# Performance work log

Hardware: AMD Instinct MI355X
Metric: run time of the kernel (lower is better)

The kernel has to match this reference:

```python
import jax, jax.numpy as jnp
import numpy as np

NH = 16  # matches init kwarg nh


def setup_inputs() -> dict:
    key = jax.random.key(0)
    k1, k2 = jax.random.split(key)
    b, S, T = 4, 4096, 4096
    x = jax.random.normal(k1, (b, S, 1), dtype=jnp.float32)
    coords_rel = jax.random.normal(k2, (2, b, S, T), dtype=jnp.float32)
    return {"x": x, "coords_rel": coords_rel}


def reference(x, coords_rel):
    # coords_rel: [2, b, S, T]; x: [b, S, 1]
    d = jnp.sqrt(coords_rel[0] ** 2 + coords_rel[1] ** 2)            # [b, S, T]
    # torch.topk(d, NH, dim=1, largest=False): smallest NH along source dim, ascending
    neg_vals, idx = jax.lax.top_k(jnp.transpose(-d, (0, 2, 1)), NH)  # [b, T, NH]
    dist_abs = jnp.transpose(-neg_vals, (0, 2, 1))                   # [b, NH, T]
    indices = jnp.transpose(idx, (0, 2, 1))                          # [b, NH, T]
    b, nh, t = dist_abs.shape
    w = 1.0 / (dist_abs + 1e-15) ** 2                                # [b, nh, t]
    denom = w.sum(axis=2)                                            # [b, nh] (sum over t, as in source)
    # faithful reproduction of torch .view(t,b,nh) raw reinterpretation + broadcast divide + .view(b,t,nh)
    w = (w.reshape(t, b, nh) / denom).reshape(b, t, nh)              # [b, t, nh]
    S = x.shape[1]
    idx_btn = indices.reshape(b, t, nh)                              # raw reshape, matches torch .view
    # gather: out[i,j,k] = x[i, idx[i,j,k], 0]  (x.repeat over last dim makes all columns equal)
    xg = jnp.take_along_axis(jnp.broadcast_to(x, (b, S, nh)), idx_btn, axis=1)  # [b, t, nh]
    out = (xg * w).sum(axis=2)                                       # [b, t]
    return out[..., None]                                            # [b, t, 1]
```

## Files before the change

kernel.cpp:

```cpp
#include <hip/hip_runtime.h>

#define B_ 4
#define S_ 4096
#define T_ 4096
#define NH_ 16
#define CPB 32
#define CPW 2
#define ROWS 64
#define NTILE (S_ / ROWS)
#define LDSP 33
#define NCG (T_ / CPB)

typedef unsigned long long u64;

__global__ __launch_bounds__(1024, 8) void topk_scan(
    const float* __restrict__ coords,
    float* __restrict__ outW,
    int*   __restrict__ outI,
    float* __restrict__ partials)
{
    __shared__ float lds0[ROWS * LDSP];
    __shared__ float lds1[ROWS * LDSP];
    __shared__ float red[16 * NH_];

    const int bid  = blockIdx.x;
    const int b    = bid >> 7;
    const int c0   = (bid & (NCG - 1)) * CPB;
    const int tid  = threadIdx.x;
    const int w    = tid >> 6;
    const int lane = tid & 63;

    const size_t plane = (size_t)B_ * S_ * T_;
    const int stid = tid & 511;
    const int srow = stid >> 3;
    const int scol = (stid & 7) * 4;
    const float* gp = coords + (size_t)b * S_ * T_ + (size_t)srow * T_ + (c0 + scol)
                    + (tid >= 512 ? plane : (size_t)0);
    float* ldsw = (tid >= 512 ? lds1 : lds0) + srow * LDSP + scol;

    float lv[CPW]; int li[CPW]; float tau[CPW];
#pragma unroll
    for (int cc = 0; cc < CPW; ++cc) {
        lv[cc]  = __int_as_float(0x7f800000);
        li[cc]  = 0;
        tau[cc] = __int_as_float(0x7f800000);
    }

    float4 v4 = *(const float4*)gp;

#pragma unroll 1
    for (int k = 0; k < NTILE; ++k) {
        __syncthreads();
        ldsw[0] = v4.x; ldsw[1] = v4.y; ldsw[2] = v4.z; ldsw[3] = v4.w;
        if (k + 1 < NTILE)
            v4 = *(const float4*)(gp + (size_t)(k + 1) * ROWS * T_);
        __syncthreads();

#pragma unroll
        for (int cc = 0; cc < CPW; ++cc) {
            const int col = w * CPW + cc;
            const float dx = lds0[lane * LDSP + col];
            const float dy = lds1[lane * LDSP + col];
            const float d2 = __fadd_rn(__fmul_rn(dx, dx), __fmul_rn(dy, dy));
            u64 m = __ballot(d2 < tau[cc]);
            while (m) {
                const int src = __ffsll(m) - 1;
                m &= m - 1;
                const float cd = __shfl(d2, src);
                const int   ci = k * ROWS + src;
                const unsigned pm = (unsigned)__ballot(lv[cc] <= cd) & 0xFFFFu;
                const int p = __popc(pm);
                const float uv = __shfl_up(lv[cc], 1);
                const int   ui = __shfl_up(li[cc], 1);
                const bool here  = (lane == p);
                const bool shift = (lane > p) && (lane < NH_);
                lv[cc] = here ? cd : (shift ? uv : lv[cc]);
                li[cc] = here ? ci : (shift ? ui : li[cc]);
                tau[cc] = __shfl(lv[cc], NH_ - 1);
                m &= __ballot(d2 < tau[cc]);
            }
        }
    }

    float dsum = 0.f;
#pragma unroll
    for (int cc = 0; cc < CPW; ++cc) {
        const int t = c0 + w * CPW + cc;
        if (lane < NH_) {
            const float d = sqrtf(lv[cc]) + 1e-15f;
            const float wv = 1.0f / (d * d);
            outW[((size_t)b * T_ + t) * NH_ + lane] = wv;
            outI[((size_t)b * T_ + t) * NH_ + lane] = li[cc];
            dsum += wv;
        }
    }
    if (lane < NH_) red[w * NH_ + lane] = dsum;
    __syncthreads();
    if (tid < NH_) {
        float s = 0.f;
#pragma unroll
        for (int q = 0; q < 16; ++q) s += red[q * NH_ + tid];
        partials[(size_t)bid * NH_ + tid] = s;
    }
}

__global__ __launch_bounds__(64) void denom_reduce(
    const float* __restrict__ partials, float* __restrict__ denom)
{
    const int q = threadIdx.x;
    const int b = q >> 4, j = q & 15;
    float s = 0.f;
    for (int g = 0; g < NCG; ++g)
        s += partials[(size_t)(b * NCG + g) * NH_ + j];
    denom[q] = s;
}

__global__ __launch_bounds__(256) void out_kernel(
    const float* __restrict__ x,
    const float* __restrict__ outW,
    const int*   __restrict__ outI,
    const float* __restrict__ denom,
    float* __restrict__ out)
{
    const int gid = blockIdx.x * 256 + threadIdx.x;
    const int i = gid >> 12;
    const int j = gid & 4095;
    const int ih = j >> 8;
    const size_t base = ((size_t)i * T_ + (size_t)(j & 255) * NH_) * NH_ + ih;
    const int dq = (j & 3) * NH_;
    float acc = 0.f;
#pragma unroll
    for (int k = 0; k < NH_; ++k) {
        float w  = outW[base + (size_t)k * NH_];
        int   id = outI[base + (size_t)k * NH_];
        acc += x[i * S_ + id] * w / denom[dq + k];
    }
    out[gid] = acc;
}

extern "C" void kernel_launch(void* const* d_in, const int* in_sizes, int n_in,
                              void* d_out, int out_size, void* d_ws, size_t ws_size,
                              hipStream_t stream) {
    const float* x      = (const float*)d_in[0];
    const float* coords = (const float*)d_in[1];
    float* out = (float*)d_out;

    float* outW     = (float*)d_ws;
    int*   outI     = (int*)(outW + (size_t)B_ * T_ * NH_);
    float* partials = (float*)(outI + (size_t)B_ * T_ * NH_);
    float* denom    = partials + (size_t)(B_ * NCG) * NH_;

    topk_scan   <<<B_ * NCG,      1024, 0, stream>>>(coords, outW, outI, partials);
    denom_reduce<<<1,             64,   0, stream>>>(partials, denom);
    out_kernel  <<<B_ * T_ / 256, 256,  0, stream>>>(x, outW, outI, denom, out);
}
```

Baseline: 155.3 us.

## Double-buffer LDS tiles in topk scan and parallelize denominator reduction

Result: faster. 152.1 us (-2.1%).

```diff
diff --git a/kernel.cpp b/kernel.cpp
--- a/kernel.cpp
+++ b/kernel.cpp
@@ -19,8 +19,7 @@
     int*   __restrict__ outI,
     float* __restrict__ partials)
 {
-    __shared__ float lds0[ROWS * LDSP];
-    __shared__ float lds1[ROWS * LDSP];
+    __shared__ float lds[2][2][ROWS * LDSP];
     __shared__ float red[16 * NH_];
 
     const int bid  = blockIdx.x;
@@ -34,9 +33,11 @@
     const int stid = tid & 511;
     const int srow = stid >> 3;
     const int scol = (stid & 7) * 4;
+    const int pl   = (tid >= 512) ? 1 : 0;
     const float* gp = coords + (size_t)b * S_ * T_ + (size_t)srow * T_ + (c0 + scol)
-                    + (tid >= 512 ? plane : (size_t)0);
-    float* ldsw = (tid >= 512 ? lds1 : lds0) + srow * LDSP + scol;
+                    + (pl ? plane : (size_t)0);
+    float* w0 = &lds[0][pl][srow * LDSP + scol];
+    float* w1 = &lds[1][pl][srow * LDSP + scol];
 
     float lv[CPW]; int li[CPW]; float tau[CPW];
 #pragma unroll
@@ -46,21 +47,27 @@
         tau[cc] = __int_as_float(0x7f800000);
     }
 
-    float4 v4 = *(const float4*)gp;
+    float4 r4 = *(const float4*)gp;
+    w0[0] = r4.x; w0[1] = r4.y; w0[2] = r4.z; w0[3] = r4.w;
+    r4 = *(const float4*)(gp + (size_t)ROWS * T_);
+    __syncthreads();
 
 #pragma unroll 1
     for (int k = 0; k < NTILE; ++k) {
-        __syncthreads();
-        ldsw[0] = v4.x; ldsw[1] = v4.y; ldsw[2] = v4.z; ldsw[3] = v4.w;
-        if (k + 1 < NTILE)
-            v4 = *(const float4*)(gp + (size_t)(k + 1) * ROWS * T_);
-        __syncthreads();
+        if (k + 1 < NTILE) {
+            float* wb = (k & 1) ? w0 : w1;
+            wb[0] = r4.x; wb[1] = r4.y; wb[2] = r4.z; wb[3] = r4.w;
+        }
+        if (k + 2 < NTILE)
+            r4 = *(const float4*)(gp + (size_t)(k + 2) * ROWS * T_);
 
+        const float* rb0 = lds[k & 1][0];
+        const float* rb1 = lds[k & 1][1];
 #pragma unroll
         for (int cc = 0; cc < CPW; ++cc) {
             const int col = w * CPW + cc;
-            const float dx = lds0[lane * LDSP + col];
-            const float dy = lds1[lane * LDSP + col];
+            const float dx = rb0[lane * LDSP + col];
+            const float dy = rb1[lane * LDSP + col];
             const float d2 = __fadd_rn(__fmul_rn(dx, dx), __fmul_rn(dy, dy));
             u64 m = __ballot(d2 < tau[cc]);
             while (m) {
@@ -80,6 +87,7 @@
                 m &= __ballot(d2 < tau[cc]);
             }
         }
+        __syncthreads();
     }
 
     float dsum = 0.f;
@@ -104,15 +112,20 @@
     }
 }
 
-__global__ __launch_bounds__(64) void denom_reduce(
+__global__ __launch_bounds__(128) void denom_reduce(
     const float* __restrict__ partials, float* __restrict__ denom)
 {
-    const int q = threadIdx.x;
+    const int q = blockIdx.x;
     const int b = q >> 4, j = q & 15;
-    float s = 0.f;
-    for (int g = 0; g < NCG; ++g)
-        s += partials[(size_t)(b * NCG + g) * NH_ + j];
-    denom[q] = s;
+    const int g = threadIdx.x;
+    __shared__ float sm[128];
+    sm[g] = partials[(size_t)(b * NCG + g) * NH_ + j];
+    __syncthreads();
+    for (int s = 64; s > 0; s >>= 1) {
+        if (g < s) sm[g] += sm[g + s];
+        __syncthreads();
+    }
+    if (g == 0) denom[q] = sm[0];
 }
 
 __global__ __launch_bounds__(256) void out_kernel(
@@ -151,6 +164,6 @@
     float* denom    = partials + (size_t)(B_ * NCG) * NH_;
 
     topk_scan   <<<B_ * NCG,      1024, 0, stream>>>(coords, outW, outI, partials);
-    denom_reduce<<<1,             64,   0, stream>>>(partials, denom);
+    denom_reduce<<<64,            128,  0, stream>>>(partials, denom);
     out_kernel  <<<B_ * T_ / 256, 256,  0, stream>>>(x, outW, outI, denom, out);
 }
```

## Split top-k scan across source spans with merge kernel and double-buffered LDS

Applied to the files above, without the earlier changes.

Measured after the change: 212.9 us. 1.37x slower.

```diff
diff --git a/kernel.cpp b/kernel.cpp
--- a/kernel.cpp
+++ b/kernel.cpp
@@ -4,39 +4,42 @@
 #define S_ 4096
 #define T_ 4096
 #define NH_ 16
-#define CPB 32
-#define CPW 2
+#define CPB 64
+#define CPW 4
 #define ROWS 64
-#define NTILE (S_ / ROWS)
-#define LDSP 33
+#define SSPAN 2048
+#define NSPAN 2
+#define NT (SSPAN / ROWS)
+#define LDSP 65
 #define NCG (T_ / CPB)
 
 typedef unsigned long long u64;
 
 __global__ __launch_bounds__(1024, 8) void topk_scan(
     const float* __restrict__ coords,
-    float* __restrict__ outW,
-    int*   __restrict__ outI,
-    float* __restrict__ partials)
-{
-    __shared__ float lds0[ROWS * LDSP];
-    __shared__ float lds1[ROWS * LDSP];
-    __shared__ float red[16 * NH_];
+    float* __restrict__ pv,
+    unsigned short* __restrict__ pi)
+{
+    __shared__ float lds[2][ROWS * LDSP];
 
     const int bid  = blockIdx.x;
     const int b    = bid >> 7;
-    const int c0   = (bid & (NCG - 1)) * CPB;
+    const int rem  = bid & 127;
+    const int cgl  = rem >> 1;
+    const int span = rem & 1;
     const int tid  = threadIdx.x;
     const int w    = tid >> 6;
     const int lane = tid & 63;
 
     const size_t plane = (size_t)B_ * S_ * T_;
-    const int stid = tid & 511;
-    const int srow = stid >> 3;
-    const int scol = (stid & 7) * 4;
-    const float* gp = coords + (size_t)b * S_ * T_ + (size_t)srow * T_ + (c0 + scol)
-                    + (tid >= 512 ? plane : (size_t)0);
-    float* ldsw = (tid >= 512 ? lds1 : lds0) + srow * LDSP + scol;
+    const int srow = tid >> 4;
+    const int scol = (tid & 15) * 4;
+    const int c0   = cgl * CPB;
+    const int s0   = span * SSPAN;
+    const float* g0 = coords + (size_t)b * S_ * T_ + (size_t)(s0 + srow) * T_ + (c0 + scol);
+    const float* g1 = g0 + plane;
+    float* w0 = &lds[0][srow * LDSP + scol];
+    float* w1 = &lds[1][srow * LDSP + scol];
 
     float lv[CPW]; int li[CPW]; float tau[CPW];
 #pragma unroll
@@ -46,28 +49,44 @@
         tau[cc] = __int_as_float(0x7f800000);
     }
 
-    float4 v4 = *(const float4*)gp;
+    float4 ax = *(const float4*)g0;
+    float4 ay = *(const float4*)g1;
+    w0[0] = __fadd_rn(__fmul_rn(ax.x, ax.x), __fmul_rn(ay.x, ay.x));
+    w0[1] = __fadd_rn(__fmul_rn(ax.y, ax.y), __fmul_rn(ay.y, ay.y));
+    w0[2] = __fadd_rn(__fmul_rn(ax.z, ax.z), __fmul_rn(ay.z, ay.z));
+    w0[3] = __fadd_rn(__fmul_rn(ax.w, ax.w), __fmul_rn(ay.w, ay.w));
+    ax = *(const float4*)(g0 + (size_t)ROWS * T_);
+    ay = *(const float4*)(g1 + (size_t)ROWS * T_);
+    __syncthreads();
 
 #pragma unroll 1
-    for (int k = 0; k < NTILE; ++k) {
-        __syncthreads();
-        ldsw[0] = v4.x; ldsw[1] = v4.y; ldsw[2] = v4.z; ldsw[3] = v4.w;
-        if (k + 1 < NTILE)
-            v4 = *(const float4*)(gp + (size_t)(k + 1) * ROWS * T_);
-        __syncthreads();
-
+    for (int k = 0; k < NT; ++k) {
+        if (k + 1 < NT) {
+            float* wb = (k & 1) ? w0 : w1;
+            wb[0] = __fadd_rn(__fmul_rn(ax.x, ax.x), __fmul_rn(ay.x, ay.x));
+            wb[1] = __fadd_rn(__fmul_rn(ax.y, ax.y), __fmul_rn(ay.y, ay.y));
+            wb[2] = __fadd_rn(__fmul_rn(ax.z, ax.z), __fmul_rn(ay.z, ay.z));
+            wb[3] = __fadd_rn(__fmul_rn(ax.w, ax.w), __fmul_rn(ay.w, ay.w));
+        }
+        if (k + 2 < NT) {
+            ax = *(const float4*)(g0 + (size_t)(k + 2) * ROWS * T_);
+            ay = *(const float4*)(g1 + (size_t)(k + 2) * ROWS * T_);
+        }
+
+        const float* rb = lds[k & 1];
+        float d2v[CPW];
+#pragma unroll
+        for (int cc = 0; cc < CPW; ++cc)
+            d2v[cc] = rb[lane * LDSP + (w * CPW + cc)];
 #pragma unroll
         for (int cc = 0; cc < CPW; ++cc) {
-            const int col = w * CPW + cc;
-            const float dx = lds0[lane * LDSP + col];
-            const float dy = lds1[lane * LDSP + col];
-            const float d2 = __fadd_rn(__fmul_rn(dx, dx), __fmul_rn(dy, dy));
+            const float d2 = d2v[cc];
             u64 m = __ballot(d2 < tau[cc]);
             while (m) {
                 const int src = __ffsll(m) - 1;
                 m &= m - 1;
                 const float cd = __shfl(d2, src);
-                const int   ci = k * ROWS + src;
+                const int   ci = s0 + k * ROWS + src;
                 const unsigned pm = (unsigned)__ballot(lv[cc] <= cd) & 0xFFFFu;
                 const int p = __popc(pm);
                 const float uv = __shfl_up(lv[cc], 1);
@@ -80,27 +99,68 @@
                 m &= __ballot(d2 < tau[cc]);
             }
         }
-    }
-
-    float dsum = 0.f;
+        __syncthreads();
+    }
+
 #pragma unroll
     for (int cc = 0; cc < CPW; ++cc) {
-        const int t = c0 + w * CPW + cc;
         if (lane < NH_) {
-            const float d = sqrtf(lv[cc]) + 1e-15f;
-            const float wv = 1.0f / (d * d);
-            outW[((size_t)b * T_ + t) * NH_ + lane] = wv;
-            outI[((size_t)b * T_ + t) * NH_ + lane] = li[cc];
-            dsum += wv;
-        }
-    }
-    if (lane < NH_) red[w * NH_ + lane] = dsum;
+            const size_t base = ((size_t)bid * NH_ + lane) * 64 + (w * CPW + cc);
+            pv[base] = lv[cc];
+            pi[base] = (unsigned short)li[cc];
+        }
+    }
+}
+
+__global__ __launch_bounds__(256) void topk_merge(
+    const float* __restrict__ pv, const unsigned short* __restrict__ pi,
+    float* __restrict__ outW,
+    int*   __restrict__ outI,
+    float* __restrict__ partials)
+{
+    __shared__ float red[NH_ * 257];
+
+    const int gc  = blockIdx.x * 256 + threadIdx.x;
+    const int b   = gc >> 12;
+    const int t   = gc & 4095;
+    const int cgl = t >> 6;
+    const int cl  = t & 63;
+    const int bid0 = ((b << 6) | cgl) << 1;
+
+    float cv[NH_]; int ci[NH_];
+#pragma unroll
+    for (int j = 0; j < NH_; ++j) { cv[j] = __int_as_float(0x7f800000); ci[j] = 0; }
+
+    for (int sp = 0; sp < NSPAN; ++sp) {
+        const size_t base = ((size_t)(bid0 + sp) * NH_) * 64 + cl;
+        for (int j = 0; j < NH_; ++j) {
+            float v = pv[base + (size_t)j * 64];
+            if (!(v < cv[NH_ - 1])) break;
+            int vi = (int)pi[base + (size_t)j * 64];
+#pragma unroll
+            for (int q = 0; q < NH_; ++q) {
+                bool sw = v < cv[q];
+                float tv = cv[q]; int ti = ci[q];
+                cv[q] = sw ? v : tv;  ci[q] = sw ? vi : ti;
+                v = sw ? tv : v;      vi = sw ? ti : vi;
+            }
+        }
+    }
+
+    const size_t obase = (size_t)gc * NH_;
+#pragma unroll
+    for (int j = 0; j < NH_; ++j) {
+        const float d = sqrtf(cv[j]) + 1e-15f;
+        const float wv = 1.0f / (d * d);
+        outW[obase + j] = wv;
+        outI[obase + j] = ci[j];
+        red[j * 257 + threadIdx.x] = wv;
+    }
     __syncthreads();
-    if (tid < NH_) {
+    if (threadIdx.x < NH_) {
         float s = 0.f;
-#pragma unroll
-        for (int q = 0; q < 16; ++q) s += red[q * NH_ + tid];
-        partials[(size_t)bid * NH_ + tid] = s;
+        for (int i = 0; i < 256; ++i) s += red[threadIdx.x * 257 + i];
+        partials[(size_t)blockIdx.x * NH_ + threadIdx.x] = s;
     }
 }
 
@@ -110,8 +170,8 @@
     const int q = threadIdx.x;
     const int b = q >> 4, j = q & 15;
     float s = 0.f;
-    for (int g = 0; g < NCG; ++g)
-        s += partials[(size_t)(b * NCG + g) * NH_ + j];
+    for (int i = 0; i < 16; ++i)
+        s += partials[(size_t)(b * 16 + i) * NH_ + j];
     denom[q] = s;
 }
 
@@ -122,20 +182,21 @@
     const float* __restrict__ denom,
     float* __restrict__ out)
 {
-    const int gid = blockIdx.x * 256 + threadIdx.x;
-    const int i = gid >> 12;
-    const int j = gid & 4095;
+    const int gid16 = blockIdx.x * 256 + threadIdx.x;
+    const int oid = gid16 >> 4;
+    const int q   = gid16 & 15;
+    const int i = oid >> 12;
+    const int j = oid & 4095;
     const int ih = j >> 8;
     const size_t base = ((size_t)i * T_ + (size_t)(j & 255) * NH_) * NH_ + ih;
-    const int dq = (j & 3) * NH_;
-    float acc = 0.f;
-#pragma unroll
-    for (int k = 0; k < NH_; ++k) {
-        float w  = outW[base + (size_t)k * NH_];
-        int   id = outI[base + (size_t)k * NH_];
-        acc += x[i * S_ + id] * w / denom[dq + k];
-    }
-    out[gid] = acc;
+    const float w  = outW[base + (size_t)q * NH_];
+    const int   id = outI[base + (size_t)q * NH_];
+    float v = x[i * S_ + id] * w / denom[(j & 3) * NH_ + q];
+    v += __shfl_xor(v, 1);
+    v += __shfl_xor(v, 2);
+    v += __shfl_xor(v, 4);
+    v += __shfl_xor(v, 8);
+    if (q == 0) out[oid] = v;
 }
 
 extern "C" void kernel_launch(void* const* d_in, const int* in_sizes, int n_in,
@@ -145,12 +206,16 @@
     const float* coords = (const float*)d_in[1];
     float* out = (float*)d_out;
 
-    float* outW     = (float*)d_ws;
-    int*   outI     = (int*)(outW + (size_t)B_ * T_ * NH_);
-    float* partials = (float*)(outI + (size_t)B_ * T_ * NH_);
-    float* denom    = partials + (size_t)(B_ * NCG) * NH_;
-
-    topk_scan   <<<B_ * NCG,      1024, 0, stream>>>(coords, outW, outI, partials);
-    denom_reduce<<<1,             64,   0, stream>>>(partials, denom);
-    out_kernel  <<<B_ * T_ / 256, 256,  0, stream>>>(x, outW, outI, denom, out);
-}
+    const int nsb = B_ * NCG * NSPAN;
+    float*          pv       = (float*)d_ws;
+    unsigned short* pi       = (unsigned short*)(pv + (size_t)nsb * NH_ * 64);
+    float*          outW     = (float*)(pi + (size_t)nsb * NH_ * 64);
+    int*            outI     = (int*)(outW + (size_t)B_ * T_ * NH_);
+    float*          partials = (float*)(outI + (size_t)B_ * T_ * NH_);
+    float*          denom    = partials + (size_t)64 * NH_;
+
+    topk_scan   <<<nsb,                1024, 0, stream>>>(coords, pv, pi);
+    topk_merge  <<<B_ * T_ / 256,      256,  0, stream>>>(pv, pi, outW, outI, partials);
+    denom_reduce<<<1,                  64,   0, stream>>>(partials, denom);
+    out_kernel  <<<B_ * T_ * 16 / 256, 256,  0, stream>>>(x, outW, outI, denom, out);
+}
```
